# Performance work log

Hardware: AMD Instinct MI355X
Metric: run time of the kernel (lower is better)

## Reference

```python
import jax, jax.numpy as jnp
import numpy as np

N = 100000  # nodes
E = 1600000  # edges

def gcn_layer(x, W, b, src, tgt, ew):
    # support = x @ W + b ; messages gathered at src, weighted scatter-sum into tgt
    h = x @ W + b                      # [N, F_out]
    msg = h[src] * ew[:, None]         # [E, F_out]
    return jax.ops.segment_sum(msg, tgt, num_segments=N)  # [N, F_out]

def setup_inputs() -> dict:
    key = jax.random.key(0)
    ks = jax.random.split(key, 12)
    nfeat, nhid, nclass = 256, 128, 40
    x = jax.random.normal(ks[0], (N, nfeat), dtype=jnp.float32)
    src = jax.random.randint(ks[1], (E,), 0, N)
    tgt = jax.random.randint(ks[2], (E,), 0, N)
    edge_weight = jax.random.uniform(ks[3], (E,), dtype=jnp.float32)
    def w(k, fi, fo):
        return jax.random.normal(k, (fi, fo), dtype=jnp.float32) / np.sqrt(fi)
    return {
        "x": x, "src": src, "tgt": tgt, "edge_weight": edge_weight,
        "W0": w(ks[4], nfeat, nhid), "b0": jnp.zeros((nhid,), jnp.float32),
        "W1": w(ks[5], nhid, nhid),  "b1": jnp.zeros((nhid,), jnp.float32),
        "W2": w(ks[6], nhid, nhid),  "b2": jnp.zeros((nhid,), jnp.float32),
        "W3": w(ks[7], nhid, nclass),"b3": jnp.zeros((nclass,), jnp.float32),
    }

def reference(x, src, tgt, edge_weight, W0, b0, W1, b1, W2, b2, W3, b3):
    # RESK2 with nlayers=4, eval mode (dropout = identity).
    # x0 = relu(gc0); r = x0; x1 = relu(gc1); x2 = relu(gc2) + r; out = log_softmax(gc3)
    x0 = jax.nn.relu(gcn_layer(x, W0, b0, src, tgt, edge_weight))
    r = x0
    x1 = jax.nn.relu(gcn_layer(x0, W1, b1, src, tgt, edge_weight))
    x2 = jax.nn.relu(gcn_layer(x1, W2, b2, src, tgt, edge_weight)) + r
    logits = gcn_layer(x2, W3, b3, src, tgt, edge_weight)
    return jax.nn.log_softmax(logits, axis=1)
```

## Files before the change

kernel.cpp:

```cpp
#include <hip/hip_runtime.h>
#include <hip/hip_bf16.h>


typedef __attribute__((ext_vector_type(8))) short short8;
typedef __attribute__((ext_vector_type(4))) float float4v;

#if defined(__has_builtin)
#if __has_builtin(__builtin_amdgcn_fdot2_f32_bf16)
#define HAVE_DOT2 1
typedef __attribute__((ext_vector_type(2))) __bf16 bf16x2;
#endif
#endif

#define SC_SHIFT 8
#define SC_NODES 256
#define FILL_CAP 12288
#define PAD_HEADROOM 4096
#define SRC_MASK 0x1FFFF

static __device__ __forceinline__ float bf2f_lo(unsigned int v) {
    return __uint_as_float(v << 16);
}
static __device__ __forceinline__ float bf2f_hi(unsigned int v) {
    return __uint_as_float(v & 0xffff0000u);
}
static __device__ __forceinline__ unsigned short f2bf(float f) {
    unsigned int u = __float_as_uint(f);
    u = (u + 0x7fffu + ((u >> 16) & 1u)) >> 16;
    return (unsigned short)u;
}
static __device__ __forceinline__ unsigned int packbf(float a, float b) {
    return (unsigned int)f2bf(a) | ((unsigned int)f2bf(b) << 16);
}

static __device__ __forceinline__ float dotp(unsigned int h2, unsigned int w2,
                                             float acc) {
#ifdef HAVE_DOT2
    return __builtin_amdgcn_fdot2_f32_bf16(__builtin_bit_cast(bf16x2, h2),
                                           __builtin_bit_cast(bf16x2, w2), acc,
                                           false);
#else
    return fmaf(bf2f_lo(h2), bf2f_lo(w2), fmaf(bf2f_hi(h2), bf2f_hi(w2), acc));
#endif
}

static __device__ __forceinline__ void acc8p(float* acc, uint4 v,
                                             unsigned int wlo, unsigned int whi) {
    acc[0] = dotp(v.x, wlo, acc[0]);
    acc[1] = dotp(v.x, whi, acc[1]);
    acc[2] = dotp(v.y, wlo, acc[2]);
    acc[3] = dotp(v.y, whi, acc[3]);
    acc[4] = dotp(v.z, wlo, acc[4]);
    acc[5] = dotp(v.z, whi, acc[5]);
    acc[6] = dotp(v.w, wlo, acc[6]);
    acc[7] = dotp(v.w, whi, acc[7]);
}
static __device__ __forceinline__ void acc4p(float* acc, uint2 v,
                                             unsigned int wlo, unsigned int whi) {
    acc[0] = dotp(v.x, wlo, acc[0]);
    acc[1] = dotp(v.x, whi, acc[1]);
    acc[2] = dotp(v.y, wlo, acc[2]);
    acc[3] = dotp(v.y, whi, acc[3]);
}

__global__ __launch_bounds__(256) void k_count(const int* __restrict__ tgt,
                                               int* __restrict__ chunkTot,
                                               int E, int NSC) {
    __shared__ int hist[512];
    const int tid = threadIdx.x;
    hist[tid] = 0;
    hist[tid + 256] = 0;
    __syncthreads();
#pragma unroll
    for (int r = 0; r < 4; r++) {
        int e = blockIdx.x * 4096 + r * 1024 + tid * 4;
        if (e + 3 < E) {
            int4 tv = *(const int4*)&tgt[e];
            atomicAdd(&hist[tv.x >> SC_SHIFT], 1);
            atomicAdd(&hist[tv.y >> SC_SHIFT], 1);
            atomicAdd(&hist[tv.z >> SC_SHIFT], 1);
            atomicAdd(&hist[tv.w >> SC_SHIFT], 1);
        } else {
            for (int j = 0; j < 4; j++)
                if (e + j < E) atomicAdd(&hist[tgt[e + j] >> SC_SHIFT], 1);
        }
    }
    __syncthreads();
    for (int i = tid; i < NSC; i += 256) {
        int c = hist[i];
        if (c) atomicAdd(&chunkTot[i], c);
    }
}

__global__ __launch_bounds__(512) void k_scanB(const int* __restrict__ chunkTot,
                                               int* __restrict__ chunkStart,
                                               int* __restrict__ chunkCur,
                                               int E, int NSC) {
    __shared__ int sm[512];
    const int tid = threadIdx.x;
    int v = (tid < NSC) ? chunkTot[tid] : 0;
    sm[tid] = v;
    __syncthreads();
    for (int off = 1; off < 512; off <<= 1) {
        int t = (tid >= off) ? sm[tid - off] : 0;
        __syncthreads();
        sm[tid] += t;
        __syncthreads();
    }
    int excl = sm[tid] - v;
    if (tid < NSC) {
        chunkStart[tid] = excl;
        chunkCur[tid * 32] = excl;
    }
    if (tid == 0) chunkStart[NSC] = E;
}

__global__ __launch_bounds__(512) void k_bucket(const int* __restrict__ src,
                                                const int* __restrict__ tgt,
                                                const float* __restrict__ ew,
                                                int* __restrict__ chunkCur,
                                                unsigned int* __restrict__ st_pw,
                                                unsigned char* __restrict__ st_t8,
                                                int E) {
    __shared__ int cnt[512];
    __shared__ int rk[512];
    __shared__ int bbase[512];
    const int tid = threadIdx.x;
    cnt[tid] = 0;
    rk[tid] = 0;
    __syncthreads();

    int t16[16];
    unsigned int p16[16];
#pragma unroll
    for (int r = 0; r < 4; r++) {
        int e = blockIdx.x * 8192 + r * 2048 + tid * 4;
        if (e + 3 < E) {
            int4 tv = *(const int4*)&tgt[e];
            int4 sv = *(const int4*)&src[e];
            float4 wv = *(const float4*)&ew[e];
            t16[r * 4 + 0] = tv.x; t16[r * 4 + 1] = tv.y;
            t16[r * 4 + 2] = tv.z; t16[r * 4 + 3] = tv.w;
            p16[r * 4 + 0] = ((unsigned int)f2bf(wv.x) << 17) | (unsigned int)sv.x;
            p16[r * 4 + 1] = ((unsigned int)f2bf(wv.y) << 17) | (unsigned int)sv.y;
            p16[r * 4 + 2] = ((unsigned int)f2bf(wv.z) << 17) | (unsigned int)sv.z;
            p16[r * 4 + 3] = ((unsigned int)f2bf(wv.w) << 17) | (unsigned int)sv.w;
        } else {
            for (int j = 0; j < 4; j++) {
                int ee = e + j;
                t16[r * 4 + j] = (ee < E) ? tgt[ee] : -1;
                p16[r * 4 + j] = (ee < E)
                    ? (((unsigned int)f2bf(ew[ee]) << 17) | (unsigned int)src[ee])
                    : 0u;
            }
        }
    }
#pragma unroll
    for (int j = 0; j < 16; j++)
        if (t16[j] >= 0) atomicAdd(&cnt[t16[j] >> SC_SHIFT], 1);
    __syncthreads();
    {
        int c = cnt[tid];
        bbase[tid] = c ? atomicAdd(&chunkCur[tid * 32], c) : 0;
    }
    __syncthreads();
#pragma unroll
    for (int j = 0; j < 16; j++) {
        if (t16[j] >= 0) {
            int c = t16[j] >> SC_SHIFT;
            int pos = bbase[c] + atomicAdd(&rk[c], 1);
            st_pw[pos] = p16[j];
            st_t8[pos] = (unsigned char)(t16[j] & (SC_NODES - 1));
        }
    }
}

__global__ __launch_bounds__(256) void k_fill2(const unsigned int* __restrict__ st_pw,
                                               const unsigned char* __restrict__ st_t8,
                                               const int* __restrict__ chunkStart,
                                               int* __restrict__ rowBeg,
                                               int* __restrict__ rowEnd,
                                               unsigned int* __restrict__ perm,
                                               int N, int NSC) {
    __shared__ int lsc[SC_NODES];
    __shared__ int lcur[SC_NODES];
    __shared__ unsigned int ledge[FILL_CAP];
    const int tid = threadIdx.x;
    const int b = blockIdx.x;
    const int n0 = b << SC_SHIFT;
    const int nlocal = min(SC_NODES, N - n0);
    const int sstart = chunkStart[b];
    const int send = chunkStart[b + 1];
    const int pstart = (sstart + b * PAD_HEADROOM + 15) & ~15;

    lsc[tid] = 0;
    __syncthreads();
    for (int e = sstart + tid; e < send; e += 256)
        atomicAdd(&lsc[st_t8[e]], 1);
    __syncthreads();
    int deg = lsc[tid];
    int pdeg = (deg + 15) & ~15;
    __syncthreads();
    lsc[tid] = pdeg;
    __syncthreads();
    for (int off = 1; off < 256; off <<= 1) {
        int t = (tid >= off) ? lsc[tid - off] : 0;
        __syncthreads();
        lsc[tid] += t;
        __syncthreads();
    }
    const int ptotal = lsc[SC_NODES - 1];
    int pexcl = lsc[tid] - pdeg;
    if (tid < nlocal) {
        rowBeg[n0 + tid] = pstart + pexcl;
        rowEnd[n0 + tid] = pstart + pexcl + pdeg;
    }
    lcur[tid] = pexcl;
    __syncthreads();

    if (ptotal <= FILL_CAP) {
        for (int i = tid; i < ptotal; i += 256) ledge[i] = 0u;
        __syncthreads();
        for (int e = sstart + tid; e < send; e += 256) {
            int lt = st_t8[e];
            int pos = atomicAdd(&lcur[lt], 1);
            ledge[pos] = st_pw[e];
        }
        __syncthreads();
        for (int i = tid; i < ptotal; i += 256) perm[pstart + i] = ledge[i];
    } else {
        for (int i = tid; i < ptotal; i += 256) perm[pstart + i] = 0u;
        __syncthreads();
        for (int e = sstart + tid; e < send; e += 256) {
            int lt = st_t8[e];
            int pos = atomicAdd(&lcur[lt], 1);
            perm[pstart + pos] = st_pw[e];
        }
    }
}

__global__ __launch_bounds__(256) void k_wtrans_all(
    const float* __restrict__ W0, const float* __restrict__ W1,
    const float* __restrict__ W2, const float* __restrict__ W3,
    unsigned short* __restrict__ Wt0, unsigned short* __restrict__ Wt1,
    unsigned short* __restrict__ Wt2, unsigned short* __restrict__ Wt3,
    int* __restrict__ chunkTot) {
    int idx = blockIdx.x * 256 + threadIdx.x;
    if (idx < 512) chunkTot[idx] = 0;
    if (idx < 32768) {
        int c = idx >> 8, k = idx & 255;
        Wt0[idx] = f2bf(W0[k * 128 + c]);
    } else if (idx < 49152) {
        int i = idx - 32768;
        int c = i >> 7, k = i & 127;
        Wt1[i] = f2bf(W1[k * 128 + c]);
    } else if (idx < 65536) {
        int i = idx - 49152;
        int c = i >> 7, k = i & 127;
        Wt2[i] = f2bf(W2[k * 128 + c]);
    } else if (idx < 71680) {
        int i = idx - 65536;
        int c = i >> 7, k = i & 127;
        Wt3[i] = (c < 40) ? f2bf(W3[k * 40 + c]) : 0;
    }
}

template <int K, int AF32>
__global__ __launch_bounds__(256) void k_gemm_mfma(const void* __restrict__ Av,
                                                   const unsigned short* __restrict__ Wt,
                                                   const float* __restrict__ bias,
                                                   unsigned short* __restrict__ C, int N) {
    __shared__ union {
        struct {
            unsigned short As[64 * 40];
            unsigned short Bs[128 * 40];
        } s;
        unsigned short Cs[64 * 136];
    } u;
    __shared__ float bsh[128];
    const unsigned short* A16 = (const unsigned short*)Av;
    const float* A32 = (const float*)Av;
    const int tid = threadIdx.x;
    const int wave = tid >> 6, lane = tid & 63;
    const int quad = lane >> 4, l15 = lane & 15;
    const int rowBase = blockIdx.x * 64;

    if (tid < 128) bsh[tid] = bias[tid];

    const int r0 = tid >> 2, kc0 = tid & 3;
    const int rB1 = r0, rB2 = r0 + 64;
    int rg0 = rowBase + r0;
    rg0 = rg0 < N ? rg0 : N - 1;

    uint4 pa, pb0, pb1;
    auto load_step = [&](int k0) {
        if (AF32) {
            float4 f0 = *(const float4*)&A32[(size_t)rg0 * K + k0 + kc0 * 8];
            float4 f1 = *(const float4*)&A32[(size_t)rg0 * K + k0 + kc0 * 8 + 4];
            pa.x = packbf(f0.x, f0.y);
            pa.y = packbf(f0.z, f0.w);
            pa.z = packbf(f1.x, f1.y);
            pa.w = packbf(f1.z, f1.w);
        } else {
            pa = *(const uint4*)&A16[(size_t)rg0 * K + k0 + kc0 * 8];
        }
        pb0 = *(const uint4*)&Wt[(size_t)rB1 * K + k0 + kc0 * 8];
        pb1 = *(const uint4*)&Wt[(size_t)rB2 * K + k0 + kc0 * 8];
    };

    const float4v z = {0.f, 0.f, 0.f, 0.f};
    float4v acc[8];
#pragma unroll
    for (int j = 0; j < 8; j++) acc[j] = z;

    load_step(0);
    for (int k0 = 0; k0 < K; k0 += 32) {
        *(uint4*)&u.s.As[r0 * 40 + kc0 * 8] = pa;
        *(uint4*)&u.s.Bs[rB1 * 40 + kc0 * 8] = pb0;
        *(uint4*)&u.s.Bs[rB2 * 40 + kc0 * 8] = pb1;
        __syncthreads();
        if (k0 + 32 < K) load_step(k0 + 32);

        short8 a = *(const short8*)&u.s.As[(wave * 16 + l15) * 40 + quad * 8];
#pragma unroll
        for (int c = 0; c < 8; c++) {
            short8 b = *(const short8*)&u.s.Bs[(c * 16 + l15) * 40 + quad * 8];
            acc[c] = __builtin_amdgcn_mfma_f32_16x16x32_bf16(b, a, acc[c], 0, 0, 0);
        }
        __syncthreads();
    }

#pragma unroll
    for (int c = 0; c < 8; c++) {
        int colBase = c * 16 + quad * 4;
        float4 bv = *(const float4*)&bsh[colBase];
        uint2 o;
        o.x = packbf(acc[c][0] + bv.x, acc[c][1] + bv.y);
        o.y = packbf(acc[c][2] + bv.z, acc[c][3] + bv.w);
        *(uint2*)&u.Cs[(wave * 16 + l15) * 136 + colBase] = o;
    }
    __syncthreads();
#pragma unroll
    for (int i = 0; i < 4; i++) {
        int flat = i * 256 + tid;
        int row = flat >> 4, q = flat & 15;
        int grow = rowBase + row;
        if (grow < N) {
            uint4 v = *(const uint4*)&u.Cs[row * 136 + q * 8];
            *(uint4*)&C[(size_t)grow * 128 + q * 8] = v;
        }
    }
}

__global__ __launch_bounds__(256) void k_gemm40_mfma(const unsigned short* __restrict__ A,
                                                     const unsigned short* __restrict__ Wt3,
                                                     const float* __restrict__ bias,
                                                     unsigned short* __restrict__ C, int N) {
    __shared__ union {
        struct {
            unsigned short As[64 * 40];
            unsigned short Bs[48 * 136];
        } s;
        unsigned short Cs[64 * 72];
    } u;
    __shared__ float bsh[64];
    const int tid = threadIdx.x;
    const int wave = tid >> 6, lane = tid & 63;
    const int quad = lane >> 4, l15 = lane & 15;
    const int rowBase = blockIdx.x * 64;

    if (tid < 64) bsh[tid] = (tid < 40) ? bias[tid] : 0.f;

    const int r0 = tid >> 2, kc0 = tid & 3;
    int rg0 = rowBase + r0;
    rg0 = rg0 < N ? rg0 : N - 1;

    for (int t = tid; t < 48 * 16; t += 256) {
        int r = t >> 4, kc = t & 15;
        uint4 v = *(const uint4*)&Wt3[r * 128 + kc * 8];
        *(uint4*)&u.s.Bs[r * 136 + kc * 8] = v;
    }

    uint4 pa;
    auto load_step = [&](int k0) {
        pa = *(const uint4*)&A[(size_t)rg0 * 128 + k0 + kc0 * 8];
    };

    const float4v z = {0.f, 0.f, 0.f, 0.f};
    float4v acc[3];
#pragma unroll
    for (int j = 0; j < 3; j++) acc[j] = z;

    load_step(0);
    for (int k0 = 0; k0 < 128; k0 += 32) {
        *(uint4*)&u.s.As[r0 * 40 + kc0 * 8] = pa;
        __syncthreads();
        if (k0 + 32 < 128) load_step(k0 + 32);

        short8 a = *(const short8*)&u.s.As[(wave * 16 + l15) * 40 + quad * 8];
#pragma unroll
        for (int c = 0; c < 3; c++) {
            short8 b = *(const short8*)&u.s.Bs[(c * 16 + l15) * 136 + k0 + quad * 8];
            acc[c] = __builtin_amdgcn_mfma_f32_16x16x32_bf16(b, a, acc[c], 0, 0, 0);
        }
        __syncthreads();
    }

#pragma unroll
    for (int c = 0; c < 4; c++) {
        int colBase = c * 16 + quad * 4;
        uint2 o;
        if (c < 3) {
            float4 bv = *(const float4*)&bsh[colBase];
            o.x = packbf(acc[c][0] + bv.x, acc[c][1] + bv.y);
            o.y = packbf(acc[c][2] + bv.z, acc[c][3] + bv.w);
        } else {
            o.x = 0u;
            o.y = 0u;
        }
        *(uint2*)&u.Cs[(wave * 16 + l15) * 72 + colBase] = o;
    }
    __syncthreads();
#pragma unroll
    for (int i = 0; i < 2; i++) {
        int flat = i * 256 + tid;
        int row = flat >> 3, q = flat & 7;
        int grow = rowBase + row;
        if (grow < N) {
            uint4 v = *(const uint4*)&u.Cs[row * 72 + q * 8];
            *(uint4*)&C[(size_t)grow * 64 + q * 8] = v;
        }
    }
}

__global__ __launch_bounds__(256) void k_agg128(const unsigned short* __restrict__ h,
                                                const int* __restrict__ rowBeg,
                                                const int* __restrict__ rowEnd,
                                                const unsigned int* __restrict__ perm,
                                                const unsigned short* __restrict__ resid,
                                                unsigned short* __restrict__ out, int N) {
    int node = (blockIdx.x * 256 + threadIdx.x) >> 6;
    if (node >= N) return;
    const int lane = threadIdx.x & 63;
    const int g = lane >> 4, l = lane & 15;
    const int beg = rowBeg[node], end = rowEnd[node];

    float acc[8] = {};
    for (int base = beg; base < end; base += 16) {
        uint4 pv = *(const uint4*)&perm[base + g * 4];
        unsigned int wl0 = pv.x >> 17, wh0 = wl0 << 16;
        unsigned int wl1 = pv.y >> 17, wh1 = wl1 << 16;
        unsigned int wl2 = pv.z >> 17, wh2 = wl2 << 16;
        unsigned int wl3 = pv.w >> 17, wh3 = wl3 << 16;
        uint4 a0 = *(const uint4*)&h[(size_t)(pv.x & SRC_MASK) * 128 + l * 8];
        uint4 a1 = *(const uint4*)&h[(size_t)(pv.y & SRC_MASK) * 128 + l * 8];
        uint4 a2 = *(const uint4*)&h[(size_t)(pv.z & SRC_MASK) * 128 + l * 8];
        uint4 a3 = *(const uint4*)&h[(size_t)(pv.w & SRC_MASK) * 128 + l * 8];
        acc8p(acc, a0, wl0, wh0);
        acc8p(acc, a1, wl1, wh1);
        acc8p(acc, a2, wl2, wh2);
        acc8p(acc, a3, wl3, wh3);
    }

#pragma unroll
    for (int i = 0; i < 8; i++) {
        acc[i] += __shfl_xor(acc[i], 16);
        acc[i] += __shfl_xor(acc[i], 32);
    }

    if (g == 0) {
#pragma unroll
        for (int i = 0; i < 8; i++) acc[i] = fmaxf(acc[i], 0.f);
        if (resid) {
            uint4 rv = *(const uint4*)&resid[(size_t)node * 128 + l * 8];
            acc[0] += bf2f_lo(rv.x); acc[1] += bf2f_hi(rv.x);
            acc[2] += bf2f_lo(rv.y); acc[3] += bf2f_hi(rv.y);
            acc[4] += bf2f_lo(rv.z); acc[5] += bf2f_hi(rv.z);
            acc[6] += bf2f_lo(rv.w); acc[7] += bf2f_hi(rv.w);
        }
        uint4 o;
        o.x = packbf(acc[0], acc[1]);
        o.y = packbf(acc[2], acc[3]);
        o.z = packbf(acc[4], acc[5]);
        o.w = packbf(acc[6], acc[7]);
        *(uint4*)&out[(size_t)node * 128 + l * 8] = o;
    }
}

__global__ __launch_bounds__(256) void k_agg40_lsm(const unsigned short* __restrict__ h,
                                                   const int* __restrict__ rowBeg,
                                                   const int* __restrict__ rowEnd,
                                                   const unsigned int* __restrict__ perm,
                                                   float* __restrict__ out, int N) {
    int node = (blockIdx.x * 256 + threadIdx.x) >> 6;
    if (node >= N) return;
    const int lane = threadIdx.x & 63;
    const int g = lane >> 4, l = lane & 15;
    const int beg = rowBeg[node], end = rowEnd[node];
    const int lc = l < 10 ? l : 0;

    float acc[4] = {};
    for (int base = beg; base < end; base += 16) {
        uint4 pv = *(const uint4*)&perm[base + g * 4];
        unsigned int wl0 = pv.x >> 17, wh0 = wl0 << 16;
        unsigned int wl1 = pv.y >> 17, wh1 = wl1 << 16;
        unsigned int wl2 = pv.z >> 17, wh2 = wl2 << 16;
        unsigned int wl3 = pv.w >> 17, wh3 = wl3 << 16;
        uint2 a0 = *(const uint2*)&h[(size_t)(pv.x & SRC_MASK) * 64 + lc * 4];
        uint2 a1 = *(const uint2*)&h[(size_t)(pv.y & SRC_MASK) * 64 + lc * 4];
        uint2 a2 = *(const uint2*)&h[(size_t)(pv.z & SRC_MASK) * 64 + lc * 4];
        uint2 a3 = *(const uint2*)&h[(size_t)(pv.w & SRC_MASK) * 64 + lc * 4];
        acc4p(acc, a0, wl0, wh0);
        acc4p(acc, a1, wl1, wh1);
        acc4p(acc, a2, wl2, wh2);
        acc4p(acc, a3, wl3, wh3);
    }
#pragma unroll
    for (int i = 0; i < 4; i++) {
        acc[i] += __shfl_xor(acc[i], 16);
        acc[i] += __shfl_xor(acc[i], 32);
    }

    bool vf = l < 10;
    float m = vf ? fmaxf(fmaxf(acc[0], acc[1]), fmaxf(acc[2], acc[3]))
                 : -__builtin_inff();
#pragma unroll
    for (int off = 1; off < 16; off <<= 1) m = fmaxf(m, __shfl_xor(m, off));
    float s = vf ? (expf(acc[0] - m) + expf(acc[1] - m) +
                    expf(acc[2] - m) + expf(acc[3] - m))
                 : 0.f;
#pragma unroll
    for (int off = 1; off < 16; off <<= 1) s += __shfl_xor(s, off);
    float ls = m + logf(s);
    if (g == 0 && vf) {
        float4 o = make_float4(acc[0] - ls, acc[1] - ls, acc[2] - ls, acc[3] - ls);
        *(float4*)&out[(size_t)node * 40 + l * 4] = o;
    }
}

extern "C" void kernel_launch(void* const* d_in, const int* in_sizes, int n_in,
                              void* d_out, int out_size, void* d_ws, size_t ws_size,
                              hipStream_t stream) {
    const float* x  = (const float*)d_in[0];
    const int*   src = (const int*)d_in[1];
    const int*   tgt = (const int*)d_in[2];
    const float* ew  = (const float*)d_in[3];
    const float* W0 = (const float*)d_in[4];
    const float* b0 = (const float*)d_in[5];
    const float* W1 = (const float*)d_in[6];
    const float* b1 = (const float*)d_in[7];
    const float* W2 = (const float*)d_in[8];
    const float* b2 = (const float*)d_in[9];
    const float* W3 = (const float*)d_in[10];
    const float* b3 = (const float*)d_in[11];

    const int N = in_sizes[0] / 256;
    const int E = in_sizes[1];
    const int NSC = (N + SC_NODES - 1) >> SC_SHIFT;

    char* ws = (char*)d_ws;
    size_t off = 0;
    auto alloc = [&](size_t bytes) -> void* {
        void* p = ws + off;
        off = (off + bytes + 255) & ~(size_t)255;
        return p;
    };
    unsigned short* XCb = (unsigned short*)alloc((size_t)N * 128 * 2);
    size_t hbytes = (size_t)N * 128 * 2;
    size_t sbytes = (size_t)E * 5 + 256;
    char* hbuf = (char*)alloc(hbytes > sbytes ? hbytes : sbytes);
    unsigned short* Hb = (unsigned short*)hbuf;
    unsigned int* st_pw = (unsigned int*)hbuf;
    unsigned char* st_t8 = (unsigned char*)(hbuf + (size_t)E * 4);
    char* buf1 = (char*)alloc((size_t)N * 128 * 2);
    unsigned short* XAb  = (unsigned short*)buf1;
    unsigned short* H40b = (unsigned short*)buf1;
    unsigned short* XBb  = (unsigned short*)alloc((size_t)N * 128 * 2);
    int*   rowBeg    = (int*)alloc((size_t)(N + 1) * 4);
    int*   rowEnd    = (int*)alloc((size_t)(N + 1) * 4);
    int*   chunkTot  = (int*)alloc(512 * 4);
    int*   chunkStart= (int*)alloc(520 * 4);
    int*   chunkCur  = (int*)alloc(512 * 32 * 4);
    unsigned int* perm = (unsigned int*)alloc(((size_t)E + (size_t)(NSC + 1) * PAD_HEADROOM) * 4);
    unsigned short* Wt0 = (unsigned short*)alloc(256 * 128 * 2);
    unsigned short* Wt1 = (unsigned short*)alloc(128 * 128 * 2);
    unsigned short* Wt2 = (unsigned short*)alloc(128 * 128 * 2);
    unsigned short* Wt3 = (unsigned short*)alloc(48 * 128 * 2);
    (void)ws_size;

    float* logits = (float*)d_out;

    k_wtrans_all<<<(71680 + 255) / 256, 256, 0, stream>>>(W0, W1, W2, W3,
                                                          Wt0, Wt1, Wt2, Wt3,
                                                          chunkTot);
    k_count<<<(E + 4095) / 4096, 256, 0, stream>>>(tgt, chunkTot, E, NSC);
    k_scanB<<<1, 512, 0, stream>>>(chunkTot, chunkStart, chunkCur, E, NSC);
    k_bucket<<<(E + 8191) / 8192, 512, 0, stream>>>(src, tgt, ew, chunkCur,
                                                    st_pw, st_t8, E);
    k_fill2<<<NSC, 256, 0, stream>>>(st_pw, st_t8, chunkStart, rowBeg, rowEnd,
                                     perm, N, NSC);

    const int gGemm = (N + 63) / 64;
    const int gWave = (N + 3) / 4;

    k_gemm_mfma<256, 1><<<gGemm, 256, 0, stream>>>(x, Wt0, b0, Hb, N);
    k_agg128<<<gWave, 256, 0, stream>>>(Hb, rowBeg, rowEnd, perm, nullptr, XAb, N);
    k_gemm_mfma<128, 0><<<gGemm, 256, 0, stream>>>(XAb, Wt1, b1, Hb, N);
    k_agg128<<<gWave, 256, 0, stream>>>(Hb, rowBeg, rowEnd, perm, nullptr, XBb, N);
    k_gemm_mfma<128, 0><<<gGemm, 256, 0, stream>>>(XBb, Wt2, b2, Hb, N);
    k_agg128<<<gWave, 256, 0, stream>>>(Hb, rowBeg, rowEnd, perm, XAb, XCb, N);
    k_gemm40_mfma<<<gGemm, 256, 0, stream>>>(XCb, Wt3, b3, H40b, N);
    k_agg40_lsm<<<gWave, 256, 0, stream>>>(H40b, rowBeg, rowEnd, perm, logits, N);
}
```

Before: 490.7 us.

## Software-pipeline gather loads in aggregation kernels and pad rows to 32 edges

The aggregation loops now process 32 edges per iteration and prefetch the next batch of perm entries and gathered feature rows while computing on the current batch. This doubles the loads in flight to hide gather latency. To let whole 32-edge steps run without bounds checks, per-node edge lists are padded to multiples of 32 and the per-block headroom is doubled. The extra padding adds zero-weight edges, which means more wasted gathers, and the double buffering raises register pressure and may lower occupancy.

```diff
diff --git a/kernel.cpp b/kernel.cpp
--- a/kernel.cpp
+++ b/kernel.cpp
@@ -15,7 +15,7 @@
 #define SC_SHIFT 8
 #define SC_NODES 256
 #define FILL_CAP 12288
-#define PAD_HEADROOM 4096
+#define PAD_HEADROOM 8192
 #define SRC_MASK 0x1FFFF
 
 static __device__ __forceinline__ float bf2f_lo(unsigned int v) {
@@ -61,6 +61,40 @@
     acc[1] = dotp(v.x, whi, acc[1]);
     acc[2] = dotp(v.y, wlo, acc[2]);
     acc[3] = dotp(v.y, whi, acc[3]);
+}
+
+static __device__ __forceinline__ void load4x16(const unsigned short* __restrict__ h,
+                                                uint4 pv, int l, uint4* d) {
+    d[0] = *(const uint4*)&h[(size_t)(pv.x & SRC_MASK) * 128 + l * 8];
+    d[1] = *(const uint4*)&h[(size_t)(pv.y & SRC_MASK) * 128 + l * 8];
+    d[2] = *(const uint4*)&h[(size_t)(pv.z & SRC_MASK) * 128 + l * 8];
+    d[3] = *(const uint4*)&h[(size_t)(pv.w & SRC_MASK) * 128 + l * 8];
+}
+static __device__ __forceinline__ void dot4x16(float* acc, uint4 pv,
+                                               const uint4* a) {
+    unsigned int wl0 = pv.x >> 17, wl1 = pv.y >> 17;
+    unsigned int wl2 = pv.z >> 17, wl3 = pv.w >> 17;
+    acc8p(acc, a[0], wl0, wl0 << 16);
+    acc8p(acc, a[1], wl1, wl1 << 16);
+    acc8p(acc, a[2], wl2, wl2 << 16);
+    acc8p(acc, a[3], wl3, wl3 << 16);
+}
+
+static __device__ __forceinline__ void load4x8(const unsigned short* __restrict__ h,
+                                               uint4 pv, int lc, uint2* d) {
+    d[0] = *(const uint2*)&h[(size_t)(pv.x & SRC_MASK) * 64 + lc * 4];
+    d[1] = *(const uint2*)&h[(size_t)(pv.y & SRC_MASK) * 64 + lc * 4];
+    d[2] = *(const uint2*)&h[(size_t)(pv.z & SRC_MASK) * 64 + lc * 4];
+    d[3] = *(const uint2*)&h[(size_t)(pv.w & SRC_MASK) * 64 + lc * 4];
+}
+static __device__ __forceinline__ void dot4x8(float* acc, uint4 pv,
+                                              const uint2* a) {
+    unsigned int wl0 = pv.x >> 17, wl1 = pv.y >> 17;
+    unsigned int wl2 = pv.z >> 17, wl3 = pv.w >> 17;
+    acc4p(acc, a[0], wl0, wl0 << 16);
+    acc4p(acc, a[1], wl1, wl1 << 16);
+    acc4p(acc, a[2], wl2, wl2 << 16);
+    acc4p(acc, a[3], wl3, wl3 << 16);
 }
 
 __global__ __launch_bounds__(256) void k_count(const int* __restrict__ tgt,
@@ -191,7 +225,7 @@
     const int nlocal = min(SC_NODES, N - n0);
     const int sstart = chunkStart[b];
     const int send = chunkStart[b + 1];
-    const int pstart = (sstart + b * PAD_HEADROOM + 15) & ~15;
+    const int pstart = (sstart + b * PAD_HEADROOM + 31) & ~31;
 
     lsc[tid] = 0;
     __syncthreads();
@@ -199,7 +233,7 @@
         atomicAdd(&lsc[st_t8[e]], 1);
     __syncthreads();
     int deg = lsc[tid];
-    int pdeg = (deg + 15) & ~15;
+    int pdeg = (deg + 31) & ~31;
     __syncthreads();
     lsc[tid] = pdeg;
     __syncthreads();
@@ -446,20 +480,30 @@
     const int beg = rowBeg[node], end = rowEnd[node];
 
     float acc[8] = {};
-    for (int base = beg; base < end; base += 16) {
-        uint4 pv = *(const uint4*)&perm[base + g * 4];
-        unsigned int wl0 = pv.x >> 17, wh0 = wl0 << 16;
-        unsigned int wl1 = pv.y >> 17, wh1 = wl1 << 16;
-        unsigned int wl2 = pv.z >> 17, wh2 = wl2 << 16;
-        unsigned int wl3 = pv.w >> 17, wh3 = wl3 << 16;
-        uint4 a0 = *(const uint4*)&h[(size_t)(pv.x & SRC_MASK) * 128 + l * 8];
-        uint4 a1 = *(const uint4*)&h[(size_t)(pv.y & SRC_MASK) * 128 + l * 8];
-        uint4 a2 = *(const uint4*)&h[(size_t)(pv.z & SRC_MASK) * 128 + l * 8];
-        uint4 a3 = *(const uint4*)&h[(size_t)(pv.w & SRC_MASK) * 128 + l * 8];
-        acc8p(acc, a0, wl0, wh0);
-        acc8p(acc, a1, wl1, wh1);
-        acc8p(acc, a2, wl2, wh2);
-        acc8p(acc, a3, wl3, wh3);
+    if (beg < end) {
+        uint4 pcur0 = *(const uint4*)&perm[beg + g * 4];
+        uint4 pcur1 = *(const uint4*)&perm[beg + 16 + g * 4];
+        uint4 hcur[8];
+        load4x16(h, pcur0, l, hcur);
+        load4x16(h, pcur1, l, hcur + 4);
+        for (int base = beg + 32;; base += 32) {
+            bool more = base < end;
+            uint4 pnx0, pnx1;
+            uint4 hnx[8];
+            if (more) {
+                pnx0 = *(const uint4*)&perm[base + g * 4];
+                pnx1 = *(const uint4*)&perm[base + 16 + g * 4];
+                load4x16(h, pnx0, l, hnx);
+                load4x16(h, pnx1, l, hnx + 4);
+            }
+            dot4x16(acc, pcur0, hcur);
+            dot4x16(acc, pcur1, hcur + 4);
+            if (!more) break;
+            pcur0 = pnx0;
+            pcur1 = pnx1;
+#pragma unroll
+            for (int i = 0; i < 8; i++) hcur[i] = hnx[i];
+        }
     }
 
 #pragma unroll
@@ -500,20 +544,30 @@
     const int lc = l < 10 ? l : 0;
 
     float acc[4] = {};
-    for (int base = beg; base < end; base += 16) {
-        uint4 pv = *(const uint4*)&perm[base + g * 4];
-        unsigned int wl0 = pv.x >> 17, wh0 = wl0 << 16;
-        unsigned int wl1 = pv.y >> 17, wh1 = wl1 << 16;
-        unsigned int wl2 = pv.z >> 17, wh2 = wl2 << 16;
-        unsigned int wl3 = pv.w >> 17, wh3 = wl3 << 16;
-        uint2 a0 = *(const uint2*)&h[(size_t)(pv.x & SRC_MASK) * 64 + lc * 4];
-        uint2 a1 = *(const uint2*)&h[(size_t)(pv.y & SRC_MASK) * 64 + lc * 4];
-        uint2 a2 = *(const uint2*)&h[(size_t)(pv.z & SRC_MASK) * 64 + lc * 4];
-        uint2 a3 = *(const uint2*)&h[(size_t)(pv.w & SRC_MASK) * 64 + lc * 4];
-        acc4p(acc, a0, wl0, wh0);
-        acc4p(acc, a1, wl1, wh1);
-        acc4p(acc, a2, wl2, wh2);
-        acc4p(acc, a3, wl3, wh3);
+    if (beg < end) {
+        uint4 pcur0 = *(const uint4*)&perm[beg + g * 4];
+        uint4 pcur1 = *(const uint4*)&perm[beg + 16 + g * 4];
+        uint2 hcur[8];
+        load4x8(h, pcur0, lc, hcur);
+        load4x8(h, pcur1, lc, hcur + 4);
+        for (int base = beg + 32;; base += 32) {
+            bool more = base < end;
+            uint4 pnx0, pnx1;
+            uint2 hnx[8];
+            if (more) {
+                pnx0 = *(const uint4*)&perm[base + g * 4];
+                pnx1 = *(const uint4*)&perm[base + 16 + g * 4];
+                load4x8(h, pnx0, lc, hnx);
+                load4x8(h, pnx1, lc, hnx + 4);
+            }
+            dot4x8(acc, pcur0, hcur);
+            dot4x8(acc, pcur1, hcur + 4);
+            if (!more) break;
+            pcur0 = pnx0;
+            pcur1 = pnx1;
+#pragma unroll
+            for (int i = 0; i < 8; i++) hcur[i] = hnx[i];
+        }
     }
 #pragma unroll
     for (int i = 0; i < 4; i++) {
```

Measured after the change: 526.8 us. 1.07x slower.
